# Performance work log

Hardware: AMD Instinct MI355X
Metric: run time of the kernel (lower is better)

The kernel has to match this reference:

```python
import jax, jax.numpy as jnp
import numpy as np

HEAD_DIM = 128

def setup_inputs() -> dict:
    key = jax.random.key(0)
    k1, k2, k3 = jax.random.split(key, 3)
    B, Q, H, D = 1, 2048, 32, HEAD_DIM
    KV = 2048
    q = jax.random.normal(k1, (B, Q, H, D), dtype=jnp.float32)
    k = jax.random.normal(k2, (B, KV, H, D), dtype=jnp.float32)
    v = jax.random.normal(k3, (B, KV, H, D), dtype=jnp.float32)
    return {"q": q, "k": k, "v": v}

def reference(q, k, v):
    B, Q, H, D = q.shape
    KV = k.shape[1]
    scale = 1.0 / jnp.sqrt(jnp.asarray(D, dtype=q.dtype))
    # [B,H,Q,KV] scores
    scores = jnp.einsum('bqhd,bkhd->bhqk', q, k) * scale
    # causal mask: disallow j > i + (KV - Q)
    i = jnp.arange(Q)[:, None]
    j = jnp.arange(KV)[None, :]
    causal = j <= i + (KV - Q)  # [Q,KV]
    scores = jnp.where(causal[None, None], scores, -jnp.inf)
    probs = jax.nn.softmax(scores.astype(jnp.float32), axis=-1)
    out = jnp.einsum('bhqk,bkhd->bqhd', probs.astype(q.dtype), v)
    roco_score = probs.sum(axis=2)            # [B,H,KV]
    roco_sq_score = (probs ** 2).sum(axis=2)  # [B,H,KV]
    return out, roco_score, roco_sq_score
```

## Files before the change

kernel.cpp:

```cpp
#include <hip/hip_runtime.h>
#include <hip/hip_bf16.h>

typedef unsigned short u16;
typedef __attribute__((ext_vector_type(8))) short bf16x8;
typedef __attribute__((ext_vector_type(4))) float f32x4;

#define NH   32
#define HD   128
#define SEQ  2048
#define BQ   64
#define BK   64

#define VT_OFF 16384
#define PS_OFF 32768

__device__ __forceinline__ int vt_key(int d) { return (d & 7) ^ ((d >> 3) & 7); }

__device__ __forceinline__ u16 f2b(float x) {
  __hip_bfloat16 hb = __float2bfloat16(x);
  return *(u16*)&hb;
}

__device__ __forceinline__ bf16x8 cvt8(const float* src) {
  float4 a = *(const float4*)(src);
  float4 b = *(const float4*)(src + 4);
  u16 t[8];
  t[0] = f2b(a.x); t[1] = f2b(a.y); t[2] = f2b(a.z); t[3] = f2b(a.w);
  t[4] = f2b(b.x); t[5] = f2b(b.y); t[6] = f2b(b.z); t[7] = f2b(b.w);
  return *(bf16x8*)t;
}

__device__ __forceinline__ bf16x8 cvt8s(const float* src, float sc) {
  float4 a = *(const float4*)(src);
  float4 b = *(const float4*)(src + 4);
  u16 t[8];
  t[0] = f2b(a.x * sc); t[1] = f2b(a.y * sc); t[2] = f2b(a.z * sc); t[3] = f2b(a.w * sc);
  t[4] = f2b(b.x * sc); t[5] = f2b(b.y * sc); t[6] = f2b(b.z * sc); t[7] = f2b(b.w * sc);
  return *(bf16x8*)t;
}

__device__ __forceinline__ void dma16(const u16* g, u16* l) {
  __builtin_amdgcn_global_load_lds(
      (const __attribute__((address_space(1))) void*)g,
      (__attribute__((address_space(3))) void*)l, 16, 0, 0);
}

__global__ __launch_bounds__(256)
void prep(const float* __restrict__ K, const float* __restrict__ V,
          u16* __restrict__ Kb, u16* __restrict__ Vtb) {
  __shared__ __align__(16) u16 T[64 * 136];
  int b = (int)blockIdx.x;
  int tid = (int)threadIdx.x;
  if (b < 4096) {
    size_t i = (size_t)b * 256 + tid;
    bf16x8 v = cvt8(K + i * 8);
    *(uint4*)(Kb + i * 8) = *(uint4*)&v;
  } else {
    b -= 4096;
    int h = b >> 5, jt = b & 31;
    #pragma unroll
    for (int it = 0; it < 4; ++it) {
      int c = tid + it * 256;
      int j = c >> 4, grp = c & 15;
      bf16x8 v = cvt8(V + ((size_t)(jt * 64 + j) * NH + h) * HD + (grp << 3));
      *(uint4*)(T + j * 136 + ((grp ^ ((j >> 3) & 7)) << 3)) = *(uint4*)&v;
    }
    __syncthreads();
    #pragma unroll
    for (int it = 0; it < 2; ++it) {
      int c = tid + it * 256;
      int d0 = (c >> 3) << 1, k = c & 7, jg = k << 3;
      int off = (((d0 >> 3) ^ k) << 3) | (d0 & 7);
      u16 lo[8], hi[8];
      #pragma unroll
      for (int e = 0; e < 8; ++e) {
        unsigned w = *(const unsigned*)(T + (jg + e) * 136 + off);
        lo[e] = (u16)w; hi[e] = (u16)(w >> 16);
      }
      *(uint4*)(Vtb + ((size_t)h * HD + d0) * SEQ + jt * 64 + jg) = *(uint4*)lo;
      *(uint4*)(Vtb + ((size_t)h * HD + d0 + 1) * SEQ + jt * 64 + jg) = *(uint4*)hi;
    }
  }
}

template <bool PRE>
__global__ __launch_bounds__(256, 2)
void attn_roco(const float* __restrict__ Qg, const float* __restrict__ Kg,
               const float* __restrict__ Vg, const u16* __restrict__ Kb,
               const u16* __restrict__ Vtb, float* __restrict__ Og,
               float* __restrict__ RS) {
  __shared__ __align__(16) u16 smem[36864];
  u16* Ks = smem;
  u16* Vt = smem + VT_OFF;
  u16* Ps = smem + PS_OFF;

  const int tid = threadIdx.x;
  const int wv  = tid >> 6;
  const int ln  = tid & 63;
  const int qd  = ln >> 4;
  const int cc  = ln & 15;

  const int h = (int)blockIdx.x & 31;
  const int pos = ((int)blockIdx.x >> 5) & 7;
  const int grp = (int)blockIdx.x >> 8;
  int qt;
  if      (grp == 0) qt = 31 - pos;
  else if (grp == 1) qt = 16 + pos;
  else if (grp == 2) qt = 15 - pos;
  else               qt = pos;

  const int qbase  = qt * BQ;
  const int ntiles = qt + 1;

  const float qsc = 0.08838834764831845f * 1.4426950408889634f;
  bf16x8 qf[4];
  {
    const float* qp = Qg + ((size_t)(qbase + wv * 16 + cc) * NH + h) * HD;
    #pragma unroll
    for (int kd = 0; kd < 4; ++kd)
      qf[kd] = cvt8s(qp + kd * 32 + qd * 8, qsc);
  }

  const int rbase = wv * 16 + qd * 4;
  float ls[4] = {0.f, 0.f, 0.f, 0.f};

  auto stageA = [&](int ta, int cur) {
    u16* ka = smem + cur * 16384;
    #pragma unroll
    for (int it = 0; it < 8; ++it) {
      int c = it * 256 + tid;
      int row = c >> 4, g = (c & 15) ^ (row & 15);
      dma16(Kb + ((size_t)(ta * 128 + row) * NH + h) * HD + (g << 3),
            ka + (size_t)c * 8);
    }
  };
  auto stageB = [&](int t, int cur) {
    u16* ks = Ks + cur * 8192;
    u16* vt = Vt + cur * 8192;
    #pragma unroll
    for (int it = 0; it < 4; ++it) {
      int c = it * 256 + tid;
      int row = c >> 4, g = (c & 15) ^ (row & 15);
      dma16(Kb + ((size_t)(t * BK + row) * NH + h) * HD + (g << 3),
            ks + (size_t)c * 8);
    }
    #pragma unroll
    for (int it = 0; it < 4; ++it) {
      int c = it * 256 + tid;
      int d = c >> 3, g = (c & 7) ^ vt_key(d);
      dma16(Vtb + ((size_t)h * HD + d) * SEQ + t * BK + (g << 3),
            vt + (size_t)c * 8);
    }
  };

  if (PRE) {
    const int ntA = (qt >> 1) + 1;
    stageA(0, 0);
    for (int ta = 0; ta < ntA; ++ta) {
      const int cur = ta & 1;
      __syncthreads();
      if (ta + 1 < ntA) stageA(ta + 1, cur ^ 1);

      const u16* ka = smem + cur * 16384;
      f32x4 S[8];
      #pragma unroll
      for (int f = 0; f < 8; ++f)
        #pragma unroll
        for (int r = 0; r < 4; ++r) S[f][r] = 0.f;

      #pragma unroll
      for (int kd = 0; kd < 4; ++kd) {
        #pragma unroll
        for (int f = 0; f < 8; ++f) {
          bf16x8 b = *(const bf16x8*)(ka + (f * 16 + cc) * 128 +
                                      (((kd * 4 + qd) ^ cc) << 3));
          S[f] = __builtin_amdgcn_mfma_f32_16x16x32_bf16(qf[kd], b, S[f], 0, 0, 0);
        }
      }

      const bool last = (ta == ntA - 1);
      #pragma unroll
      for (int r = 0; r < 4; ++r) {
        const int ig = qbase + rbase + r;
        float acc = 0.f;
        #pragma unroll
        for (int f = 0; f < 8; ++f) {
          float e = __builtin_amdgcn_exp2f(S[f][r]);
          if (last && (ta * 128 + f * 16 + cc) > ig) e = 0.f;
          acc += e;
        }
        ls[r] += acc;
      }
    }
    __syncthreads();
  } else {
    for (int t = 0; t < ntiles; ++t) {
      __syncthreads();
      #pragma unroll
      for (int it = 0; it < 4; ++it) {
        int c = tid + it * 256;
        int row = c >> 4, g = c & 15;
        bf16x8 kv = cvt8(Kg + ((size_t)(t * BK + row) * NH + h) * HD + (g << 3));
        *(uint4*)(Ks + row * 128 + ((g ^ (row & 15)) << 3)) = *(uint4*)&kv;
      }
      __syncthreads();

      f32x4 S[4];
      #pragma unroll
      for (int f = 0; f < 4; ++f)
        #pragma unroll
        for (int r = 0; r < 4; ++r) S[f][r] = 0.f;

      #pragma unroll
      for (int kd = 0; kd < 4; ++kd) {
        #pragma unroll
        for (int f = 0; f < 4; ++f) {
          bf16x8 b = *(const bf16x8*)(Ks + (f * 16 + cc) * 128 +
                                      (((kd * 4 + qd) ^ cc) << 3));
          S[f] = __builtin_amdgcn_mfma_f32_16x16x32_bf16(qf[kd], b, S[f], 0, 0, 0);
        }
      }

      const bool diag = (t == qt);
      #pragma unroll
      for (int r = 0; r < 4; ++r) {
        const int iloc = rbase + r;
        float acc = 0.f;
        #pragma unroll
        for (int f = 0; f < 4; ++f) {
          float e = __builtin_amdgcn_exp2f(S[f][r]);
          if (diag && (f * 16 + cc) > iloc) e = 0.f;
          acc += e;
        }
        ls[r] += acc;
      }
    }
  }

  float invl[4];
  #pragma unroll
  for (int r = 0; r < 4; ++r) {
    #pragma unroll
    for (int off = 1; off < 16; off <<= 1)
      ls[r] += __shfl_xor(ls[r], off);
    invl[r] = 1.f / ls[r];
  }

  f32x4 O[8];
  #pragma unroll
  for (int f = 0; f < 8; ++f)
    #pragma unroll
    for (int r = 0; r < 4; ++r) O[f][r] = 0.f;

  float* ws_s = RS + (size_t)h * SEQ;
  float* ws_q = RS + (size_t)NH * SEQ + (size_t)h * SEQ;

  if (PRE) stageB(0, 0);
  for (int t = 0; t < ntiles; ++t) {
    const int cur = PRE ? (t & 1) : 0;
    __syncthreads();
    if (PRE) {
      if (t + 1 < ntiles) stageB(t + 1, cur ^ 1);
    } else {
      #pragma unroll
      for (int it = 0; it < 4; ++it) {
        int c = tid + it * 256;
        int row = c >> 4, g = c & 15;
        bf16x8 kv = cvt8(Kg + ((size_t)(t * BK + row) * NH + h) * HD + (g << 3));
        *(uint4*)(Ks + row * 128 + ((g ^ (row & 15)) << 3)) = *(uint4*)&kv;
      }
      #pragma unroll
      for (int it = 0; it < 4; ++it) {
        int c = tid + it * 256;
        int j = c >> 4, d0 = (c & 15) << 3;
        bf16x8 v = cvt8(Vg + ((size_t)(t * BK + j) * NH + h) * HD + d0);
        u16 ev[8];
        *(uint4*)ev = *(uint4*)&v;
        #pragma unroll
        for (int e = 0; e < 8; ++e) {
          int d = d0 + e;
          Vt[d * BK + ((((j >> 3) ^ vt_key(d)) << 3)) + (j & 7)] = ev[e];
        }
      }
      __syncthreads();
    }

    const u16* ks = Ks + cur * 8192;
    const u16* vt = Vt + cur * 8192;

    f32x4 S[4];
    #pragma unroll
    for (int f = 0; f < 4; ++f)
      #pragma unroll
      for (int r = 0; r < 4; ++r) S[f][r] = 0.f;

    #pragma unroll
    for (int kd = 0; kd < 4; ++kd) {
      #pragma unroll
      for (int f = 0; f < 4; ++f) {
        bf16x8 b = *(const bf16x8*)(ks + (f * 16 + cc) * 128 +
                                    (((kd * 4 + qd) ^ cc) << 3));
        S[f] = __builtin_amdgcn_mfma_f32_16x16x32_bf16(qf[kd], b, S[f], 0, 0, 0);
      }
    }

    const bool diag = (t == qt);
    float cs[4] = {0.f, 0.f, 0.f, 0.f}, cq[4] = {0.f, 0.f, 0.f, 0.f};
    #pragma unroll
    for (int r = 0; r < 4; ++r) {
      const int iloc = rbase + r;
      const int prow = wv * 16 + qd * 4 + r;
      #pragma unroll
      for (int f = 0; f < 4; ++f) {
        float p = __builtin_amdgcn_exp2f(S[f][r]) * invl[r];
        if (diag && (f * 16 + cc) > iloc) p = 0.f;
        cs[f] += p;
        cq[f] += p * p;
        int pg = f * 2 + (cc >> 3);
        Ps[prow * 64 + ((pg ^ (prow & 7)) << 3) + (cc & 7)] = f2b(p);
      }
    }
    #pragma unroll
    for (int f = 0; f < 4; ++f) {
      cs[f] += __shfl_xor(cs[f], 16); cs[f] += __shfl_xor(cs[f], 32);
      cq[f] += __shfl_xor(cq[f], 16); cq[f] += __shfl_xor(cq[f], 32);
      if (qd == f) {
        int j = t * BK + f * 16 + cc;
        atomicAdd(ws_s + j, cs[f]);
        atomicAdd(ws_q + j, cq[f]);
      }
    }
    #pragma unroll
    for (int ks2 = 0; ks2 < 2; ++ks2) {
      bf16x8 a = *(const bf16x8*)(Ps + (wv * 16 + cc) * 64 +
                                  (((ks2 * 4 + qd) ^ (cc & 7)) << 3));
      #pragma unroll
      for (int f2 = 0; f2 < 8; ++f2) {
        int d = f2 * 16 + cc;
        int jb = ks2 * 4 + qd;
        bf16x8 b = *(const bf16x8*)(vt + d * BK + ((jb ^ vt_key(d)) << 3));
        O[f2] = __builtin_amdgcn_mfma_f32_16x16x32_bf16(a, b, O[f2], 0, 0, 0);
      }
    }
  }

  #pragma unroll
  for (int f2 = 0; f2 < 8; ++f2) {
    #pragma unroll
    for (int r = 0; r < 4; ++r) {
      int i = qbase + rbase + r;
      int d = f2 * 16 + cc;
      Og[((size_t)i * NH + h) * HD + d] = O[f2][r];
    }
  }
}

extern "C" void kernel_launch(void* const* d_in, const int* in_sizes, int n_in,
                              void* d_out, int out_size, void* d_ws, size_t ws_size,
                              hipStream_t stream) {
  (void)in_sizes; (void)n_in; (void)out_size;
  const float* Qg = (const float*)d_in[0];
  const float* Kg = (const float*)d_in[1];
  const float* Vg = (const float*)d_in[2];
  float* Og = (float*)d_out;

  const size_t roco_elems = (size_t)2 * NH * SEQ;
  const size_t tens = (size_t)SEQ * NH * HD;
  const size_t need = 2 * tens * 2;
  const bool pre = ws_size >= need;

  float* RS = Og + tens;
  (void)hipMemsetAsync(RS, 0, roco_elems * sizeof(float), stream);

  u16* Kb  = (u16*)d_ws;
  u16* Vtb = Kb + tens;

  if (pre) {
    prep<<<dim3(4096 + 1024), dim3(256), 0, stream>>>(Kg, Vg, Kb, Vtb);
    attn_roco<true><<<dim3(NH * (SEQ / BQ)), dim3(256), 0, stream>>>(
        Qg, Kg, Vg, Kb, Vtb, Og, RS);
  } else {
    attn_roco<false><<<dim3(NH * (SEQ / BQ)), dim3(256), 0, stream>>>(
        Qg, Kg, Vg, Kb, Vtb, Og, RS);
  }
}
```

Measured before the change: 230.3 us.

## Double query tile to 128 rows with 8 waves and skip fully masked causal work

The query block grows from 64 to 128 rows and the block size from 256 to 512 threads, so each staged K/V tile is reused by twice as many query rows. On the diagonal tile, waves skip score MFMAs for causally masked key groups in the row-sum pass and whole waves skip the output pass for fully masked tiles. This halves the number of blocks (512 instead of 1024) and changes the block-to-tile mapping, which may cost occupancy and load balance. Idle waves in the masked region still reach every barrier.

```diff
diff --git a/kernel.cpp b/kernel.cpp
--- a/kernel.cpp
+++ b/kernel.cpp
@@ -8,7 +8,7 @@
 #define NH   32
 #define HD   128
 #define SEQ  2048
-#define BQ   64
+#define BQ   128
 #define BK   64
 
 #define VT_OFF 16384
@@ -84,12 +84,12 @@
 }
 
 template <bool PRE>
-__global__ __launch_bounds__(256, 2)
+__global__ __launch_bounds__(512, 2)
 void attn_roco(const float* __restrict__ Qg, const float* __restrict__ Kg,
                const float* __restrict__ Vg, const u16* __restrict__ Kb,
                const u16* __restrict__ Vtb, float* __restrict__ Og,
                float* __restrict__ RS) {
-  __shared__ __align__(16) u16 smem[36864];
+  __shared__ __align__(16) u16 smem[40960];
   u16* Ks = smem;
   u16* Vt = smem + VT_OFF;
   u16* Ps = smem + PS_OFF;
@@ -101,16 +101,13 @@
   const int cc  = ln & 15;
 
   const int h = (int)blockIdx.x & 31;
-  const int pos = ((int)blockIdx.x >> 5) & 7;
-  const int grp = (int)blockIdx.x >> 8;
-  int qt;
-  if      (grp == 0) qt = 31 - pos;
-  else if (grp == 1) qt = 16 + pos;
-  else if (grp == 2) qt = 15 - pos;
-  else               qt = pos;
-
-  const int qbase  = qt * BQ;
-  const int ntiles = qt + 1;
+  const int idx = (int)blockIdx.x >> 5;
+  const int pos = idx & 7;
+  const int qt  = (idx >> 3) ? pos : 15 - pos;
+
+  const int qbase = qt * BQ;
+  const int ntB   = 2 * qt + 2;
+  const int ntA   = qt + 1;
 
   const float qsc = 0.08838834764831845f * 1.4426950408889634f;
   bf16x8 qf[4];
@@ -127,8 +124,8 @@
   auto stageA = [&](int ta, int cur) {
     u16* ka = smem + cur * 16384;
     #pragma unroll
-    for (int it = 0; it < 8; ++it) {
-      int c = it * 256 + tid;
+    for (int it = 0; it < 4; ++it) {
+      int c = it * 512 + tid;
       int row = c >> 4, g = (c & 15) ^ (row & 15);
       dma16(Kb + ((size_t)(ta * 128 + row) * NH + h) * HD + (g << 3),
             ka + (size_t)c * 8);
@@ -138,15 +135,15 @@
     u16* ks = Ks + cur * 8192;
     u16* vt = Vt + cur * 8192;
     #pragma unroll
-    for (int it = 0; it < 4; ++it) {
-      int c = it * 256 + tid;
+    for (int it = 0; it < 2; ++it) {
+      int c = it * 512 + tid;
       int row = c >> 4, g = (c & 15) ^ (row & 15);
       dma16(Kb + ((size_t)(t * BK + row) * NH + h) * HD + (g << 3),
             ks + (size_t)c * 8);
     }
     #pragma unroll
-    for (int it = 0; it < 4; ++it) {
-      int c = it * 256 + tid;
+    for (int it = 0; it < 2; ++it) {
+      int c = it * 512 + tid;
       int d = c >> 3, g = (c & 7) ^ vt_key(d);
       dma16(Vtb + ((size_t)h * HD + d) * SEQ + t * BK + (g << 3),
             vt + (size_t)c * 8);
@@ -154,7 +151,6 @@
   };
 
   if (PRE) {
-    const int ntA = (qt >> 1) + 1;
     stageA(0, 0);
     for (int ta = 0; ta < ntA; ++ta) {
       const int cur = ta & 1;
@@ -162,6 +158,7 @@
       if (ta + 1 < ntA) stageA(ta + 1, cur ^ 1);
 
       const u16* ka = smem + cur * 16384;
+      const bool last = (ta == ntA - 1);
       f32x4 S[8];
       #pragma unroll
       for (int f = 0; f < 8; ++f)
@@ -172,13 +169,14 @@
       for (int kd = 0; kd < 4; ++kd) {
         #pragma unroll
         for (int f = 0; f < 8; ++f) {
-          bf16x8 b = *(const bf16x8*)(ka + (f * 16 + cc) * 128 +
-                                      (((kd * 4 + qd) ^ cc) << 3));
-          S[f] = __builtin_amdgcn_mfma_f32_16x16x32_bf16(qf[kd], b, S[f], 0, 0, 0);
-        }
-      }
-
-      const bool last = (ta == ntA - 1);
+          if (!last || f <= wv) {
+            bf16x8 b = *(const bf16x8*)(ka + (f * 16 + cc) * 128 +
+                                        (((kd * 4 + qd) ^ cc) << 3));
+            S[f] = __builtin_amdgcn_mfma_f32_16x16x32_bf16(qf[kd], b, S[f], 0, 0, 0);
+          }
+        }
+      }
+
       #pragma unroll
       for (int r = 0; r < 4; ++r) {
         const int ig = qbase + rbase + r;
@@ -194,84 +192,87 @@
     }
     __syncthreads();
   } else {
-    for (int t = 0; t < ntiles; ++t) {
+    for (int ta = 0; ta < ntA; ++ta) {
       __syncthreads();
       #pragma unroll
       for (int it = 0; it < 4; ++it) {
-        int c = tid + it * 256;
+        int c = tid + it * 512;
+        int row = c >> 4, g = c & 15;
+        bf16x8 kv = cvt8(Kg + ((size_t)(ta * 128 + row) * NH + h) * HD + (g << 3));
+        *(uint4*)(smem + row * 128 + ((g ^ (row & 15)) << 3)) = *(uint4*)&kv;
+      }
+      __syncthreads();
+
+      const bool last = (ta == ntA - 1);
+      f32x4 S[8];
+      #pragma unroll
+      for (int f = 0; f < 8; ++f)
+        #pragma unroll
+        for (int r = 0; r < 4; ++r) S[f][r] = 0.f;
+
+      #pragma unroll
+      for (int kd = 0; kd < 4; ++kd) {
+        #pragma unroll
+        for (int f = 0; f < 8; ++f) {
+          if (!last || f <= wv) {
+            bf16x8 b = *(const bf16x8*)(smem + (f * 16 + cc) * 128 +
+                                        (((kd * 4 + qd) ^ cc) << 3));
+            S[f] = __builtin_amdgcn_mfma_f32_16x16x32_bf16(qf[kd], b, S[f], 0, 0, 0);
+          }
+        }
+      }
+
+      #pragma unroll
+      for (int r = 0; r < 4; ++r) {
+        const int ig = qbase + rbase + r;
+        float acc = 0.f;
+        #pragma unroll
+        for (int f = 0; f < 8; ++f) {
+          float e = __builtin_amdgcn_exp2f(S[f][r]);
+          if (last && (ta * 128 + f * 16 + cc) > ig) e = 0.f;
+          acc += e;
+        }
+        ls[r] += acc;
+      }
+    }
+    __syncthreads();
+  }
+
+  float invl[4];
+  #pragma unroll
+  for (int r = 0; r < 4; ++r) {
+    #pragma unroll
+    for (int off = 1; off < 16; off <<= 1)
+      ls[r] += __shfl_xor(ls[r], off);
+    invl[r] = 1.f / ls[r];
+  }
+
+  f32x4 O[8];
+  #pragma unroll
+  for (int f = 0; f < 8; ++f)
+    #pragma unroll
+    for (int r = 0; r < 4; ++r) O[f][r] = 0.f;
+
+  float* ws_s = RS + (size_t)h * SEQ;
+  float* ws_q = RS + (size_t)NH * SEQ + (size_t)h * SEQ;
+
+  if (PRE) stageB(0, 0);
+  for (int t = 0; t < ntB; ++t) {
+    const int cur = PRE ? (t & 1) : 0;
+    __syncthreads();
+    if (PRE) {
+      if (t + 1 < ntB) stageB(t + 1, cur ^ 1);
+    } else {
+      #pragma unroll
+      for (int it = 0; it < 2; ++it) {
+        int c = tid + it * 512;
         int row = c >> 4, g = c & 15;
         bf16x8 kv = cvt8(Kg + ((size_t)(t * BK + row) * NH + h) * HD + (g << 3));
         *(uint4*)(Ks + row * 128 + ((g ^ (row & 15)) << 3)) = *(uint4*)&kv;
       }
-      __syncthreads();
-
-      f32x4 S[4];
-      #pragma unroll
-      for (int f = 0; f < 4; ++f)
-        #pragma unroll
-        for (int r = 0; r < 4; ++r) S[f][r] = 0.f;
-
-      #pragma unroll
-      for (int kd = 0; kd < 4; ++kd) {
-        #pragma unroll
-        for (int f = 0; f < 4; ++f) {
-          bf16x8 b = *(const bf16x8*)(Ks + (f * 16 + cc) * 128 +
-                                      (((kd * 4 + qd) ^ cc) << 3));
-          S[f] = __builtin_amdgcn_mfma_f32_16x16x32_bf16(qf[kd], b, S[f], 0, 0, 0);
-        }
-      }
-
-      const bool diag = (t == qt);
-      #pragma unroll
-      for (int r = 0; r < 4; ++r) {
-        const int iloc = rbase + r;
-        float acc = 0.f;
-        #pragma unroll
-        for (int f = 0; f < 4; ++f) {
-          float e = __builtin_amdgcn_exp2f(S[f][r]);
-          if (diag && (f * 16 + cc) > iloc) e = 0.f;
-          acc += e;
-        }
-        ls[r] += acc;
-      }
-    }
-  }
-
-  float invl[4];
-  #pragma unroll
-  for (int r = 0; r < 4; ++r) {
-    #pragma unroll
-    for (int off = 1; off < 16; off <<= 1)
-      ls[r] += __shfl_xor(ls[r], off);
-    invl[r] = 1.f / ls[r];
-  }
-
-  f32x4 O[8];
-  #pragma unroll
-  for (int f = 0; f < 8; ++f)
-    #pragma unroll
-    for (int r = 0; r < 4; ++r) O[f][r] = 0.f;
-
-  float* ws_s = RS + (size_t)h * SEQ;
-  float* ws_q = RS + (size_t)NH * SEQ + (size_t)h * SEQ;
-
-  if (PRE) stageB(0, 0);
-  for (int t = 0; t < ntiles; ++t) {
-    const int cur = PRE ? (t & 1) : 0;
-    __syncthreads();
-    if (PRE) {
-      if (t + 1 < ntiles) stageB(t + 1, cur ^ 1);
-    } else {
-      #pragma unroll
-      for (int it = 0; it < 4; ++it) {
-        int c = tid + it * 256;
-        int row = c >> 4, g = c & 15;
-        bf16x8 kv = cvt8(Kg + ((size_t)(t * BK + row) * NH + h) * HD + (g << 3));
-        *(uint4*)(Ks + row * 128 + ((g ^ (row & 15)) << 3)) = *(uint4*)&kv;
-      }
-      #pragma unroll
-      for (int it = 0; it < 4; ++it) {
-        int c = tid + it * 256;
+      #pragma unroll
+      for (int it = 0; it < 2; ++it) {
+        int c = tid + it * 512;
         int j = c >> 4, d0 = (c & 15) << 3;
         bf16x8 v = cvt8(Vg + ((size_t)(t * BK + j) * NH + h) * HD + d0);
         u16 ev[8];
@@ -285,61 +286,65 @@
       __syncthreads();
     }
 
-    const u16* ks = Ks + cur * 8192;
-    const u16* vt = Vt + cur * 8192;
-
-    f32x4 S[4];
-    #pragma unroll
-    for (int f = 0; f < 4; ++f)
-      #pragma unroll
-      for (int r = 0; r < 4; ++r) S[f][r] = 0.f;
-
-    #pragma unroll
-    for (int kd = 0; kd < 4; ++kd) {
+    const bool wactive = (t * 64) <= (qbase + wv * 16 + 15);
+    if (wactive) {
+      const u16* ks = Ks + cur * 8192;
+      const u16* vt = Vt + cur * 8192;
+
+      f32x4 S[4];
+      #pragma unroll
+      for (int f = 0; f < 4; ++f)
+        #pragma unroll
+        for (int r = 0; r < 4; ++r) S[f][r] = 0.f;
+
+      #pragma unroll
+      for (int kd = 0; kd < 4; ++kd) {
+        #pragma unroll
+        for (int f = 0; f < 4; ++f) {
+          bf16x8 b = *(const bf16x8*)(ks + (f * 16 + cc) * 128 +
+                                      (((kd * 4 + qd) ^ cc) << 3));
+          S[f] = __builtin_amdgcn_mfma_f32_16x16x32_bf16(qf[kd], b, S[f], 0, 0, 0);
+        }
+      }
+
+      const bool diag = (t >= 2 * qt);
+      const int jb0 = (t - 2 * qt) * 64;
+      float cs[4] = {0.f, 0.f, 0.f, 0.f}, cq[4] = {0.f, 0.f, 0.f, 0.f};
+      #pragma unroll
+      for (int r = 0; r < 4; ++r) {
+        const int iloc = rbase + r;
+        const int prow = rbase + r;
+        #pragma unroll
+        for (int f = 0; f < 4; ++f) {
+          float p = __builtin_amdgcn_exp2f(S[f][r]) * invl[r];
+          if (diag && (jb0 + f * 16 + cc) > iloc) p = 0.f;
+          cs[f] += p;
+          cq[f] += p * p;
+          int pg = f * 2 + (cc >> 3);
+          Ps[prow * 64 + ((pg ^ (prow & 7)) << 3) + (cc & 7)] = f2b(p);
+        }
+      }
       #pragma unroll
       for (int f = 0; f < 4; ++f) {
-        bf16x8 b = *(const bf16x8*)(ks + (f * 16 + cc) * 128 +
-                                    (((kd * 4 + qd) ^ cc) << 3));
-        S[f] = __builtin_amdgcn_mfma_f32_16x16x32_bf16(qf[kd], b, S[f], 0, 0, 0);
-      }
-    }
-
-    const bool diag = (t == qt);
-    float cs[4] = {0.f, 0.f, 0.f, 0.f}, cq[4] = {0.f, 0.f, 0.f, 0.f};
-    #pragma unroll
-    for (int r = 0; r < 4; ++r) {
-      const int iloc = rbase + r;
-      const int prow = wv * 16 + qd * 4 + r;
-      #pragma unroll
-      for (int f = 0; f < 4; ++f) {
-        float p = __builtin_amdgcn_exp2f(S[f][r]) * invl[r];
-        if (diag && (f * 16 + cc) > iloc) p = 0.f;
-        cs[f] += p;
-        cq[f] += p * p;
-        int pg = f * 2 + (cc >> 3);
-        Ps[prow * 64 + ((pg ^ (prow & 7)) << 3) + (cc & 7)] = f2b(p);
-      }
-    }
-    #pragma unroll
-    for (int f = 0; f < 4; ++f) {
-      cs[f] += __shfl_xor(cs[f], 16); cs[f] += __shfl_xor(cs[f], 32);
-      cq[f] += __shfl_xor(cq[f], 16); cq[f] += __shfl_xor(cq[f], 32);
-      if (qd == f) {
-        int j = t * BK + f * 16 + cc;
-        atomicAdd(ws_s + j, cs[f]);
-        atomicAdd(ws_q + j, cq[f]);
-      }
-    }
-    #pragma unroll
-    for (int ks2 = 0; ks2 < 2; ++ks2) {
-      bf16x8 a = *(const bf16x8*)(Ps + (wv * 16 + cc) * 64 +
-                                  (((ks2 * 4 + qd) ^ (cc & 7)) << 3));
-      #pragma unroll
-      for (int f2 = 0; f2 < 8; ++f2) {
-        int d = f2 * 16 + cc;
-        int jb = ks2 * 4 + qd;
-        bf16x8 b = *(const bf16x8*)(vt + d * BK + ((jb ^ vt_key(d)) << 3));
-        O[f2] = __builtin_amdgcn_mfma_f32_16x16x32_bf16(a, b, O[f2], 0, 0, 0);
+        cs[f] += __shfl_xor(cs[f], 16); cs[f] += __shfl_xor(cs[f], 32);
+        cq[f] += __shfl_xor(cq[f], 16); cq[f] += __shfl_xor(cq[f], 32);
+        if (qd == f) {
+          int j = t * BK + f * 16 + cc;
+          atomicAdd(ws_s + j, cs[f]);
+          atomicAdd(ws_q + j, cq[f]);
+        }
+      }
+      #pragma unroll
+      for (int ks2 = 0; ks2 < 2; ++ks2) {
+        bf16x8 a = *(const bf16x8*)(Ps + (wv * 16 + cc) * 64 +
+                                    (((ks2 * 4 + qd) ^ (cc & 7)) << 3));
+        #pragma unroll
+        for (int f2 = 0; f2 < 8; ++f2) {
+          int d = f2 * 16 + cc;
+          int jb = ks2 * 4 + qd;
+          bf16x8 b = *(const bf16x8*)(vt + d * BK + ((jb ^ vt_key(d)) << 3));
+          O[f2] = __builtin_amdgcn_mfma_f32_16x16x32_bf16(a, b, O[f2], 0, 0, 0);
+        }
       }
     }
   }
@@ -377,10 +382,10 @@
 
   if (pre) {
     prep<<<dim3(4096 + 1024), dim3(256), 0, stream>>>(Kg, Vg, Kb, Vtb);
-    attn_roco<true><<<dim3(NH * (SEQ / BQ)), dim3(256), 0, stream>>>(
+    attn_roco<true><<<dim3(NH * (SEQ / BQ)), dim3(512), 0, stream>>>(
         Qg, Kg, Vg, Kb, Vtb, Og, RS);
   } else {
-    attn_roco<false><<<dim3(NH * (SEQ / BQ)), dim3(256), 0, stream>>>(
+    attn_roco<false><<<dim3(NH * (SEQ / BQ)), dim3(512), 0, stream>>>(
         Qg, Kg, Vg, Kb, Vtb, Og, RS);
   }
 }
```

After: 249.6 us. 8.4% more time.

## Replace LDS double-buffered DMA staging with register-prefetch single-buffer pipeline

Applied to the files above, without the earlier changes.

Direct global-to-LDS DMA loads with double-buffered shared memory are replaced by register prefetch of the next K/V tiles, which are then stored into a single LDS buffer each iteration. This shrinks shared memory from about 72KB to 40KB and drops the launch_bounds min-blocks hint, aiming for better occupancy or scheduling. The row-sum pass also skips the upper half of MFMAs on the final tile when it lies entirely beyond the causal diagonal. The cost is higher register pressure and an extra sync plus LDS store per tile.

```diff
diff --git a/kernel.cpp b/kernel.cpp
--- a/kernel.cpp
+++ b/kernel.cpp
@@ -11,8 +11,8 @@
 #define BQ   64
 #define BK   64
 
-#define VT_OFF 16384
-#define PS_OFF 32768
+#define VT_OFF 8192
+#define PS_OFF 16384
 
 __device__ __forceinline__ int vt_key(int d) { return (d & 7) ^ ((d >> 3) & 7); }
 
@@ -37,12 +37,6 @@
   t[0] = f2b(a.x * sc); t[1] = f2b(a.y * sc); t[2] = f2b(a.z * sc); t[3] = f2b(a.w * sc);
   t[4] = f2b(b.x * sc); t[5] = f2b(b.y * sc); t[6] = f2b(b.z * sc); t[7] = f2b(b.w * sc);
   return *(bf16x8*)t;
-}
-
-__device__ __forceinline__ void dma16(const u16* g, u16* l) {
-  __builtin_amdgcn_global_load_lds(
-      (const __attribute__((address_space(1))) void*)g,
-      (__attribute__((address_space(3))) void*)l, 16, 0, 0);
 }
 
 __global__ __launch_bounds__(256)
@@ -84,12 +78,12 @@
 }
 
 template <bool PRE>
-__global__ __launch_bounds__(256, 2)
+__global__ __launch_bounds__(256)
 void attn_roco(const float* __restrict__ Qg, const float* __restrict__ Kg,
                const float* __restrict__ Vg, const u16* __restrict__ Kb,
                const u16* __restrict__ Vtb, float* __restrict__ Og,
                float* __restrict__ RS) {
-  __shared__ __align__(16) u16 smem[36864];
+  __shared__ __align__(16) u16 smem[20480];
   u16* Ks = smem;
   u16* Vt = smem + VT_OFF;
   u16* Ps = smem + PS_OFF;
@@ -124,44 +118,29 @@
   const int rbase = wv * 16 + qd * 4;
   float ls[4] = {0.f, 0.f, 0.f, 0.f};
 
-  auto stageA = [&](int ta, int cur) {
-    u16* ka = smem + cur * 16384;
-    #pragma unroll
-    for (int it = 0; it < 8; ++it) {
-      int c = it * 256 + tid;
-      int row = c >> 4, g = (c & 15) ^ (row & 15);
-      dma16(Kb + ((size_t)(ta * 128 + row) * NH + h) * HD + (g << 3),
-            ka + (size_t)c * 8);
-    }
-  };
-  auto stageB = [&](int t, int cur) {
-    u16* ks = Ks + cur * 8192;
-    u16* vt = Vt + cur * 8192;
-    #pragma unroll
-    for (int it = 0; it < 4; ++it) {
-      int c = it * 256 + tid;
-      int row = c >> 4, g = (c & 15) ^ (row & 15);
-      dma16(Kb + ((size_t)(t * BK + row) * NH + h) * HD + (g << 3),
-            ks + (size_t)c * 8);
-    }
-    #pragma unroll
-    for (int it = 0; it < 4; ++it) {
-      int c = it * 256 + tid;
-      int d = c >> 3, g = (c & 7) ^ vt_key(d);
-      dma16(Vtb + ((size_t)h * HD + d) * SEQ + t * BK + (g << 3),
-            vt + (size_t)c * 8);
-    }
-  };
-
   if (PRE) {
     const int ntA = (qt >> 1) + 1;
-    stageA(0, 0);
+    uint4 ka[8];
+    auto loadA = [&](int ta) {
+      #pragma unroll
+      for (int it = 0; it < 8; ++it) {
+        int c = tid + it * 256;
+        int row = c >> 4, g = (c & 15) ^ (row & 15);
+        ka[it] = *(const uint4*)(Kb + ((size_t)(ta * 128 + row) * NH + h) * HD +
+                                 (g << 3));
+      }
+    };
+    loadA(0);
     for (int ta = 0; ta < ntA; ++ta) {
-      const int cur = ta & 1;
-      __syncthreads();
-      if (ta + 1 < ntA) stageA(ta + 1, cur ^ 1);
-
-      const u16* ka = smem + cur * 16384;
+      __syncthreads();
+      #pragma unroll
+      for (int it = 0; it < 8; ++it)
+        *(uint4*)(smem + (size_t)(tid + it * 256) * 8) = ka[it];
+      __syncthreads();
+      if (ta + 1 < ntA) loadA(ta + 1);
+
+      const bool last = (ta == ntA - 1);
+      const bool skipHi = last && !(qt & 1);
       f32x4 S[8];
       #pragma unroll
       for (int f = 0; f < 8; ++f)
@@ -172,13 +151,14 @@
       for (int kd = 0; kd < 4; ++kd) {
         #pragma unroll
         for (int f = 0; f < 8; ++f) {
-          bf16x8 b = *(const bf16x8*)(ka + (f * 16 + cc) * 128 +
-                                      (((kd * 4 + qd) ^ cc) << 3));
-          S[f] = __builtin_amdgcn_mfma_f32_16x16x32_bf16(qf[kd], b, S[f], 0, 0, 0);
-        }
-      }
-
-      const bool last = (ta == ntA - 1);
+          if (!(skipHi && f >= 4)) {
+            bf16x8 b = *(const bf16x8*)(smem + (f * 16 + cc) * 128 +
+                                        (((kd * 4 + qd) ^ cc) << 3));
+            S[f] = __builtin_amdgcn_mfma_f32_16x16x32_bf16(qf[kd], b, S[f], 0, 0, 0);
+          }
+        }
+      }
+
       #pragma unroll
       for (int r = 0; r < 4; ++r) {
         const int ig = qbase + rbase + r;
@@ -192,7 +172,6 @@
         ls[r] += acc;
       }
     }
-    __syncthreads();
   } else {
     for (int t = 0; t < ntiles; ++t) {
       __syncthreads();
@@ -255,12 +234,36 @@
   float* ws_s = RS + (size_t)h * SEQ;
   float* ws_q = RS + (size_t)NH * SEQ + (size_t)h * SEQ;
 
-  if (PRE) stageB(0, 0);
+  uint4 kr[4], vr[4];
+  auto loadB = [&](int t) {
+    #pragma unroll
+    for (int it = 0; it < 4; ++it) {
+      int c = tid + it * 256;
+      int row = c >> 4, g = (c & 15) ^ (row & 15);
+      kr[it] = *(const uint4*)(Kb + ((size_t)(t * BK + row) * NH + h) * HD +
+                               (g << 3));
+    }
+    #pragma unroll
+    for (int it = 0; it < 4; ++it) {
+      int c = tid + it * 256;
+      int d = c >> 3, g = (c & 7) ^ vt_key(d);
+      vr[it] = *(const uint4*)(Vtb + ((size_t)h * HD + d) * SEQ + t * BK +
+                               (g << 3));
+    }
+  };
+
+  if (PRE) loadB(0);
   for (int t = 0; t < ntiles; ++t) {
-    const int cur = PRE ? (t & 1) : 0;
     __syncthreads();
     if (PRE) {
-      if (t + 1 < ntiles) stageB(t + 1, cur ^ 1);
+      #pragma unroll
+      for (int it = 0; it < 4; ++it)
+        *(uint4*)(Ks + (size_t)(tid + it * 256) * 8) = kr[it];
+      #pragma unroll
+      for (int it = 0; it < 4; ++it)
+        *(uint4*)(Vt + (size_t)(tid + it * 256) * 8) = vr[it];
+      __syncthreads();
+      if (t + 1 < ntiles) loadB(t + 1);
     } else {
       #pragma unroll
       for (int it = 0; it < 4; ++it) {
@@ -285,9 +288,6 @@
       __syncthreads();
     }
 
-    const u16* ks = Ks + cur * 8192;
-    const u16* vt = Vt + cur * 8192;
-
     f32x4 S[4];
     #pragma unroll
     for (int f = 0; f < 4; ++f)
@@ -298,7 +298,7 @@
     for (int kd = 0; kd < 4; ++kd) {
       #pragma unroll
       for (int f = 0; f < 4; ++f) {
-        bf16x8 b = *(const bf16x8*)(ks + (f * 16 + cc) * 128 +
+        bf16x8 b = *(const bf16x8*)(Ks + (f * 16 + cc) * 128 +
                                     (((kd * 4 + qd) ^ cc) << 3));
         S[f] = __builtin_amdgcn_mfma_f32_16x16x32_bf16(qf[kd], b, S[f], 0, 0, 0);
       }
@@ -338,7 +338,7 @@
       for (int f2 = 0; f2 < 8; ++f2) {
         int d = f2 * 16 + cc;
         int jb = ks2 * 4 + qd;
-        bf16x8 b = *(const bf16x8*)(vt + d * BK + ((jb ^ vt_key(d)) << 3));
+        bf16x8 b = *(const bf16x8*)(Vt + d * BK + ((jb ^ vt_key(d)) << 3));
         O[f2] = __builtin_amdgcn_mfma_f32_16x16x32_bf16(a, b, O[f2], 0, 0, 0);
       }
     }
```

Measured after the change: 441.0 us. +91.4%, slower.

## Drop double-buffered async staging and alias P tile onto K shared memory

Applied to the files above, without the earlier changes.

Removes the double-buffered DMA prefetch of K and V^T tiles in both passes. Each tile is now loaded and consumed in place behind barriers, and the P staging buffer is aliased onto the K tile region, which needs an extra barrier after QK^T. This cuts shared memory from 72KB to 32KB per block and drops the occupancy hint from launch_bounds, allowing more resident blocks per CU. In exchange, global-load latency is no longer hidden by explicit prefetch and each iteration gains an extra synchronization.

```diff
diff --git a/kernel.cpp b/kernel.cpp
--- a/kernel.cpp
+++ b/kernel.cpp
@@ -11,8 +11,7 @@
 #define BQ   64
 #define BK   64
 
-#define VT_OFF 16384
-#define PS_OFF 32768
+#define VT_OFF 8192
 
 __device__ __forceinline__ int vt_key(int d) { return (d & 7) ^ ((d >> 3) & 7); }
 
@@ -84,15 +83,15 @@
 }
 
 template <bool PRE>
-__global__ __launch_bounds__(256, 2)
+__global__ __launch_bounds__(256)
 void attn_roco(const float* __restrict__ Qg, const float* __restrict__ Kg,
                const float* __restrict__ Vg, const u16* __restrict__ Kb,
                const u16* __restrict__ Vtb, float* __restrict__ Og,
                float* __restrict__ RS) {
-  __shared__ __align__(16) u16 smem[36864];
+  __shared__ __align__(16) u16 smem[16384];
   u16* Ks = smem;
   u16* Vt = smem + VT_OFF;
-  u16* Ps = smem + PS_OFF;
+  u16* Ps = smem;
 
   const int tid = threadIdx.x;
   const int wv  = tid >> 6;
@@ -124,44 +123,19 @@
   const int rbase = wv * 16 + qd * 4;
   float ls[4] = {0.f, 0.f, 0.f, 0.f};
 
-  auto stageA = [&](int ta, int cur) {
-    u16* ka = smem + cur * 16384;
-    #pragma unroll
-    for (int it = 0; it < 8; ++it) {
-      int c = it * 256 + tid;
-      int row = c >> 4, g = (c & 15) ^ (row & 15);
-      dma16(Kb + ((size_t)(ta * 128 + row) * NH + h) * HD + (g << 3),
-            ka + (size_t)c * 8);
-    }
-  };
-  auto stageB = [&](int t, int cur) {
-    u16* ks = Ks + cur * 8192;
-    u16* vt = Vt + cur * 8192;
-    #pragma unroll
-    for (int it = 0; it < 4; ++it) {
-      int c = it * 256 + tid;
-      int row = c >> 4, g = (c & 15) ^ (row & 15);
-      dma16(Kb + ((size_t)(t * BK + row) * NH + h) * HD + (g << 3),
-            ks + (size_t)c * 8);
-    }
-    #pragma unroll
-    for (int it = 0; it < 4; ++it) {
-      int c = it * 256 + tid;
-      int d = c >> 3, g = (c & 7) ^ vt_key(d);
-      dma16(Vtb + ((size_t)h * HD + d) * SEQ + t * BK + (g << 3),
-            vt + (size_t)c * 8);
-    }
-  };
-
   if (PRE) {
     const int ntA = (qt >> 1) + 1;
-    stageA(0, 0);
     for (int ta = 0; ta < ntA; ++ta) {
-      const int cur = ta & 1;
       __syncthreads();
-      if (ta + 1 < ntA) stageA(ta + 1, cur ^ 1);
-
-      const u16* ka = smem + cur * 16384;
+      #pragma unroll
+      for (int it = 0; it < 8; ++it) {
+        int c = it * 256 + tid;
+        int row = c >> 4, g = (c & 15) ^ (row & 15);
+        dma16(Kb + ((size_t)(ta * 128 + row) * NH + h) * HD + (g << 3),
+              smem + (size_t)c * 8);
+      }
+      __syncthreads();
+
       f32x4 S[8];
       #pragma unroll
       for (int f = 0; f < 8; ++f)
@@ -172,7 +146,7 @@
       for (int kd = 0; kd < 4; ++kd) {
         #pragma unroll
         for (int f = 0; f < 8; ++f) {
-          bf16x8 b = *(const bf16x8*)(ka + (f * 16 + cc) * 128 +
+          bf16x8 b = *(const bf16x8*)(smem + (f * 16 + cc) * 128 +
                                       (((kd * 4 + qd) ^ cc) << 3));
           S[f] = __builtin_amdgcn_mfma_f32_16x16x32_bf16(qf[kd], b, S[f], 0, 0, 0);
         }
@@ -192,7 +166,6 @@
         ls[r] += acc;
       }
     }
-    __syncthreads();
   } else {
     for (int t = 0; t < ntiles; ++t) {
       __syncthreads();
@@ -255,12 +228,23 @@
   float* ws_s = RS + (size_t)h * SEQ;
   float* ws_q = RS + (size_t)NH * SEQ + (size_t)h * SEQ;
 
-  if (PRE) stageB(0, 0);
   for (int t = 0; t < ntiles; ++t) {
-    const int cur = PRE ? (t & 1) : 0;
     __syncthreads();
     if (PRE) {
-      if (t + 1 < ntiles) stageB(t + 1, cur ^ 1);
+      #pragma unroll
+      for (int it = 0; it < 4; ++it) {
+        int c = it * 256 + tid;
+        int row = c >> 4, g = (c & 15) ^ (row & 15);
+        dma16(Kb + ((size_t)(t * BK + row) * NH + h) * HD + (g << 3),
+              Ks + (size_t)c * 8);
+      }
+      #pragma unroll
+      for (int it = 0; it < 4; ++it) {
+        int c = it * 256 + tid;
+        int d = c >> 3, g = (c & 7) ^ vt_key(d);
+        dma16(Vtb + ((size_t)h * HD + d) * SEQ + t * BK + (g << 3),
+              Vt + (size_t)c * 8);
+      }
     } else {
       #pragma unroll
       for (int it = 0; it < 4; ++it) {
@@ -282,11 +266,8 @@
           Vt[d * BK + ((((j >> 3) ^ vt_key(d)) << 3)) + (j & 7)] = ev[e];
         }
       }
-      __syncthreads();
-    }
-
-    const u16* ks = Ks + cur * 8192;
-    const u16* vt = Vt + cur * 8192;
+    }
+    __syncthreads();
 
     f32x4 S[4];
     #pragma unroll
@@ -298,11 +279,13 @@
     for (int kd = 0; kd < 4; ++kd) {
       #pragma unroll
       for (int f = 0; f < 4; ++f) {
-        bf16x8 b = *(const bf16x8*)(ks + (f * 16 + cc) * 128 +
+        bf16x8 b = *(const bf16x8*)(Ks + (f * 16 + cc) * 128 +
                                     (((kd * 4 + qd) ^ cc) << 3));
         S[f] = __builtin_amdgcn_mfma_f32_16x16x32_bf16(qf[kd], b, S[f], 0, 0, 0);
       }
     }
+
+    __syncthreads();
 
     const bool diag = (t == qt);
     float cs[4] = {0.f, 0.f, 0.f, 0.f}, cq[4] = {0.f, 0.f, 0.f, 0.f};
@@ -338,7 +321,7 @@
       for (int f2 = 0; f2 < 8; ++f2) {
         int d = f2 * 16 + cc;
         int jb = ks2 * 4 + qd;
-        bf16x8 b = *(const bf16x8*)(vt + d * BK + ((jb ^ vt_key(d)) << 3));
+        bf16x8 b = *(const bf16x8*)(Vt + d * BK + ((jb ^ vt_key(d)) << 3));
         O[f2] = __builtin_amdgcn_mfma_f32_16x16x32_bf16(a, b, O[f2], 0, 0, 0);
       }
     }
```

Result: slower. 239.1 us (+3.8%).
